# Performance work log

Measured on AMD Instinct MI355X. Metric: run time of the kernel, lower is better.

The kernel has to match this reference:

```python
import jax, jax.numpy as jnp
import numpy as np

T = 4096          # total packed tokens
SEG = 512         # segment length (position_ids reset every SEG)
D = 768           # hidden_size
H = 12            # num_attention_heads
DH = D // H       # head_dim = 64
THETA = 160000.0  # global_rope_theta (layer_id=0 -> global attention)


def setup_inputs() -> dict:
    key = jax.random.key(0)
    k1, k2, k3 = jax.random.split(key, 3)
    hidden_states = jax.random.normal(k1, (T, D), dtype=jnp.float32)
    # torch Linear weights stored transposed: here [in, out] for x @ W
    Wqkv = jax.random.normal(k2, (D, 3 * D), dtype=jnp.float32) / np.sqrt(D).astype(np.float32)
    Wo = jax.random.normal(k3, (D, D), dtype=jnp.float32) / np.sqrt(D).astype(np.float32)
    # packed batch: 8 segments of length SEG, position ids restart at 0
    position_ids = (jnp.arange(T, dtype=jnp.int32) % SEG)
    return {"hidden_states": hidden_states, "Wqkv": Wqkv, "Wo": Wo,
            "position_ids": position_ids}


def _neox_rope(x, pos):
    # x: [T, H, DH]; neox-style rotary over full head_dim
    half = DH // 2
    inv_freq = 1.0 / (THETA ** (jnp.arange(half, dtype=jnp.float32) * 2.0 / DH))
    freqs = pos.astype(jnp.float32)[:, None] * inv_freq[None, :]   # [T, half]
    cos = jnp.cos(freqs)[:, None, :]                               # [T, 1, half]
    sin = jnp.sin(freqs)[:, None, :]
    x1, x2 = x[..., :half], x[..., half:]
    return jnp.concatenate([x1 * cos - x2 * sin, x2 * cos + x1 * sin], axis=-1)


def reference(hidden_states, Wqkv, Wo, position_ids):
    qkv = hidden_states @ Wqkv                         # [T, 3D]
    q, k, v = jnp.split(qkv, 3, axis=-1)
    q = q.reshape(T, H, DH)
    k = k.reshape(T, H, DH)
    v = v.reshape(T, H, DH)
    q = _neox_rope(q, position_ids)
    k = _neox_rope(k, position_ids)
    # segment id per token (position_ids==0 marks a new sequence)
    seg = jnp.cumsum((position_ids == 0).astype(jnp.int32)) - 1
    mask = seg[:, None] == seg[None, :]                # block-diagonal [T, T]
    scale = 1.0 / np.sqrt(DH).astype(np.float32)
    scores = jnp.einsum('thd,shd->hts', q, k) * scale  # [H, T, T]
    scores = jnp.where(mask[None, :, :], scores, jnp.float32(-1e30))
    attn = jax.nn.softmax(scores, axis=-1)
    out = jnp.einsum('hts,shd->thd', attn, v).reshape(T, D)
    return out @ Wo
```

## Files before the change

### kernel.cpp

```cpp
#include <hip/hip_runtime.h>
#include <hip/hip_bf16.h>
#include <math.h>

#define T_TOK 4096
#define D_MODEL 768
#define H_HEADS 12
#define DH 64
#define SEG 512
#define NSEG 8
#define QKV_LD 2304

typedef __bf16 bf16x8_t __attribute__((ext_vector_type(8)));
typedef float f32x4_t __attribute__((ext_vector_type(4)));
typedef float f32x16_t __attribute__((ext_vector_type(16)));

#define GBK 64

#define FENCED_BARRIER()                         \
    do {                                         \
        __builtin_amdgcn_sched_barrier(0);       \
        __builtin_amdgcn_s_barrier();            \
        __builtin_amdgcn_sched_barrier(0);       \
    } while (0)

__device__ __forceinline__ void tconv_body(const float* __restrict__ in,
                                           __hip_bfloat16* __restrict__ out,
                                           int N, int K, int bx, int by, int tid,
                                           float (*tile)[65]) {
    const int k0 = by * 64;
    const int n0 = bx * 64;
    const int rr = tid >> 4;
    const int cc = (tid & 15) * 4;
#pragma unroll
    for (int i = 0; i < 4; ++i) {
        int r = i * 16 + rr;
        float4 v = *(const float4*)(in + (size_t)(k0 + r) * N + n0 + cc);
        tile[r][cc] = v.x; tile[r][cc + 1] = v.y; tile[r][cc + 2] = v.z; tile[r][cc + 3] = v.w;
    }
    __syncthreads();
#pragma unroll
    for (int i = 0; i < 4; ++i) {
        int n = i * 16 + rr;
        union { __hip_bfloat16 h[4]; ushort4 u; } o;
        o.h[0] = __float2bfloat16(tile[cc + 0][n]);
        o.h[1] = __float2bfloat16(tile[cc + 1][n]);
        o.h[2] = __float2bfloat16(tile[cc + 2][n]);
        o.h[3] = __float2bfloat16(tile[cc + 3][n]);
        *(ushort4*)(out + (size_t)(n0 + n) * K + k0 + cc) = o.u;
    }
}

__global__ __launch_bounds__(256) void prep_inputs(const float* __restrict__ hidden,
                                                   const float* __restrict__ Wqkv,
                                                   const float* __restrict__ Wo,
                                                   __hip_bfloat16* __restrict__ Xb,
                                                   __hip_bfloat16* __restrict__ Wqkvt,
                                                   __hip_bfloat16* __restrict__ Wot) {
    __shared__ float tile[64][65];
    const int b = blockIdx.x;
    const int tid = threadIdx.x;
    if (b < 3072) {
        int i = b * 256 + tid;
        float4 v = ((const float4*)hidden)[i];
        union { __hip_bfloat16 h[4]; ushort4 u; } o;
        o.h[0] = __float2bfloat16(v.x); o.h[1] = __float2bfloat16(v.y);
        o.h[2] = __float2bfloat16(v.z); o.h[3] = __float2bfloat16(v.w);
        ((ushort4*)Xb)[i] = o.u;
    } else if (b < 3504) {
        int lb = b - 3072;
        tconv_body(Wqkv, Wqkvt, QKV_LD, D_MODEL, lb % 36, lb / 36, tid, tile);
    } else {
        int lb = b - 3504;
        tconv_body(Wo, Wot, D_MODEL, D_MODEL, lb % 12, lb / 12, tid, tile);
    }
}

__global__ __launch_bounds__(512) void gemm_qkv_fused(const __hip_bfloat16* __restrict__ A,
                                                      const __hip_bfloat16* __restrict__ Bt,
                                                      const int* __restrict__ pos_ids,
                                                      __hip_bfloat16* __restrict__ Qb,
                                                      __hip_bfloat16* __restrict__ Kb,
                                                      __hip_bfloat16* __restrict__ Vtb) {
    __shared__ __hip_bfloat16 As[2][128 * GBK];
    __shared__ __hip_bfloat16 Bs[2][128 * GBK];
    const int tid = threadIdx.x;
    const int lane = tid & 63;
    const int wid = tid >> 6;
    const int wr = wid >> 1;
    const int wc = wid & 1;
    const int m0 = blockIdx.y * 128;
    const int n0 = blockIdx.x * 128;
    const int K = D_MODEL;

    f32x4_t acc[2][4];
#pragma unroll
    for (int i = 0; i < 2; ++i)
#pragma unroll
        for (int j = 0; j < 4; ++j) acc[i][j] = (f32x4_t){0.f, 0.f, 0.f, 0.f};

    const int lr = lane >> 3;
    const int gc = lane & 7;
    const int swzc = (gc ^ lr) << 3;
    const int fr = lane & 15;
    const int l4 = lane >> 4;
    const int fsw = fr & 7;

#define STAGE_Q(buf_, k0_)                                                            \
    do {                                                                              \
        _Pragma("unroll")                                                             \
        for (int i_ = 0; i_ < 2; ++i_) {                                              \
            const int row_ = i_ * 64 + wid * 8;                                       \
            const __hip_bfloat16* ga_ = A + (size_t)(m0 + row_ + lr) * K + (k0_) + swzc; \
            __builtin_amdgcn_global_load_lds(                                         \
                (const __attribute__((address_space(1))) void*)ga_,                   \
                (__attribute__((address_space(3))) void*)(As[buf_] + row_ * GBK), 16, 0, 0); \
            const __hip_bfloat16* gb_ = Bt + (size_t)(n0 + row_ + lr) * K + (k0_) + swzc; \
            __builtin_amdgcn_global_load_lds(                                         \
                (const __attribute__((address_space(1))) void*)gb_,                   \
                (__attribute__((address_space(3))) void*)(Bs[buf_] + row_ * GBK), 16, 0, 0); \
        }                                                                             \
    } while (0)

    const int NKT = K / GBK;
    STAGE_Q(0, 0);
    for (int kt = 0; kt < NKT; ++kt) {
        const int cur = kt & 1;
        if (kt < NKT - 1) {
            STAGE_Q(cur ^ 1, (kt + 1) * GBK);
            asm volatile("s_waitcnt vmcnt(4)" ::: "memory");
        } else {
            asm volatile("s_waitcnt vmcnt(0)" ::: "memory");
        }
        FENCED_BARRIER();
#pragma unroll
        for (int kk = 0; kk < 2; ++kk) {
            const int rg = ((kk * 4 + l4) ^ fsw) << 3;
            bf16x8_t af[2], bfr[4];
#pragma unroll
            for (int mi = 0; mi < 2; ++mi)
                af[mi] = *(const bf16x8_t*)(As[cur] + (wr * 32 + mi * 16 + fr) * GBK + rg);
#pragma unroll
            for (int ni = 0; ni < 4; ++ni)
                bfr[ni] = *(const bf16x8_t*)(Bs[cur] + (wc * 64 + ni * 16 + fr) * GBK + rg);
#pragma unroll
            for (int mi = 0; mi < 2; ++mi)
#pragma unroll
                for (int ni = 0; ni < 4; ++ni)
                    acc[mi][ni] = __builtin_amdgcn_mfma_f32_16x16x32_bf16(
                        af[mi], bfr[ni], acc[mi][ni], 0, 0, 0);
        }
        asm volatile("" ::: "memory");
        FENCED_BARRIER();
    }
#undef STAGE_Q

    const int colbase = n0 + wc * 64;
    const int chunk = colbase >> 6;
    const int part = chunk / H_HEADS;
    const int h = chunk % H_HEADS;
    const int trow0 = m0 + wr * 32;

    if (part == 2) {
        const int seg = trow0 >> 9;
        const int key0 = (trow0 & 511) + l4 * 4;
        __hip_bfloat16* vdst = Vtb + ((size_t)(h * NSEG + seg) * DH) * SEG;
#pragma unroll
        for (int mi = 0; mi < 2; ++mi)
#pragma unroll
            for (int ni = 0; ni < 4; ++ni) {
                int d = ni * 16 + fr;
                union { __hip_bfloat16 h2[4]; ushort4 u; } o;
#pragma unroll
                for (int j = 0; j < 4; ++j) o.h2[j] = __float2bfloat16(acc[mi][ni][j]);
                *(ushort4*)(vdst + (size_t)d * SEG + key0 + mi * 16) = o.u;
            }
    } else {
        __hip_bfloat16* dst = (part == 0) ? Qb : Kb;
        const float scale = (part == 0) ? 0.125f : 1.0f;
        const float if0 = powf(160000.0f, -(float)fr / 32.0f);
        const float if1 = powf(160000.0f, -(float)(16 + fr) / 32.0f);
#pragma unroll
        for (int mi = 0; mi < 2; ++mi)
#pragma unroll
            for (int j = 0; j < 4; ++j) {
                int t = trow0 + mi * 16 + l4 * 4 + j;
                float pos = (float)pos_ids[t];
                float s0, c0, s1, c1;
                sincosf(pos * if0, &s0, &c0);
                sincosf(pos * if1, &s1, &c1);
                __hip_bfloat16* op = dst + ((size_t)h * T_TOK + t) * DH;
                float x1, x2;
                x1 = acc[mi][0][j]; x2 = acc[mi][2][j];
                op[fr]      = __float2bfloat16((x1 * c0 - x2 * s0) * scale);
                op[fr + 32] = __float2bfloat16((x2 * c0 + x1 * s0) * scale);
                x1 = acc[mi][1][j]; x2 = acc[mi][3][j];
                op[16 + fr] = __float2bfloat16((x1 * c1 - x2 * s1) * scale);
                op[48 + fr] = __float2bfloat16((x2 * c1 + x1 * s1) * scale);
            }
    }
}

__global__ __launch_bounds__(256) void gemm_wo64(const __hip_bfloat16* __restrict__ A,
                                                 const __hip_bfloat16* __restrict__ Bt,
                                                 float* __restrict__ C) {
    __shared__ __hip_bfloat16 As[2][64 * GBK];
    __shared__ __hip_bfloat16 Bs[2][64 * GBK];
    const int tid = threadIdx.x;
    const int lane = tid & 63;
    const int wid = tid >> 6;
    const int wr = wid >> 1, wc = wid & 1;
    const int m0 = blockIdx.y * 64;
    const int n0 = blockIdx.x * 64;
    const int K = D_MODEL;
    const int N = D_MODEL;

    f32x4_t acc[2][2];
#pragma unroll
    for (int i = 0; i < 2; ++i)
#pragma unroll
        for (int j = 0; j < 2; ++j) acc[i][j] = (f32x4_t){0.f, 0.f, 0.f, 0.f};

    const int lr = lane >> 3;
    const int gc = lane & 7;
    const int swzc = (gc ^ lr) << 3;
    const int fr = lane & 15;
    const int l4 = lane >> 4;
    const int fsw = fr & 7;

#define STAGE_W(buf_, k0_)                                                            \
    do {                                                                              \
        _Pragma("unroll")                                                             \
        for (int i_ = 0; i_ < 2; ++i_) {                                              \
            const int row_ = i_ * 32 + wid * 8;                                       \
            const __hip_bfloat16* ga_ = A + (size_t)(m0 + row_ + lr) * K + (k0_) + swzc; \
            __builtin_amdgcn_global_load_lds(                                         \
                (const __attribute__((address_space(1))) void*)ga_,                   \
                (__attribute__((address_space(3))) void*)(As[buf_] + row_ * GBK), 16, 0, 0); \
            const __hip_bfloat16* gb_ = Bt + (size_t)(n0 + row_ + lr) * K + (k0_) + swzc; \
            __builtin_amdgcn_global_load_lds(                                         \
                (const __attribute__((address_space(1))) void*)gb_,                   \
                (__attribute__((address_space(3))) void*)(Bs[buf_] + row_ * GBK), 16, 0, 0); \
        }                                                                             \
    } while (0)

    const int NKT = K / GBK;
    STAGE_W(0, 0);
    for (int kt = 0; kt < NKT; ++kt) {
        const int cur = kt & 1;
        if (kt < NKT - 1) {
            STAGE_W(cur ^ 1, (kt + 1) * GBK);
            asm volatile("s_waitcnt vmcnt(4)" ::: "memory");
        } else {
            asm volatile("s_waitcnt vmcnt(0)" ::: "memory");
        }
        FENCED_BARRIER();
#pragma unroll
        for (int kk = 0; kk < 2; ++kk) {
            const int rg = ((kk * 4 + l4) ^ fsw) << 3;
            bf16x8_t af[2], bfr[2];
#pragma unroll
            for (int mi = 0; mi < 2; ++mi)
                af[mi] = *(const bf16x8_t*)(As[cur] + (wr * 32 + mi * 16 + fr) * GBK + rg);
#pragma unroll
            for (int ni = 0; ni < 2; ++ni)
                bfr[ni] = *(const bf16x8_t*)(Bs[cur] + (wc * 32 + ni * 16 + fr) * GBK + rg);
#pragma unroll
            for (int mi = 0; mi < 2; ++mi)
#pragma unroll
                for (int ni = 0; ni < 2; ++ni)
                    acc[mi][ni] = __builtin_amdgcn_mfma_f32_16x16x32_bf16(
                        af[mi], bfr[ni], acc[mi][ni], 0, 0, 0);
        }
        asm volatile("" ::: "memory");
        FENCED_BARRIER();
    }
#undef STAGE_W

    float* Cb = C + (size_t)(m0 + wr * 32) * N + n0 + wc * 32;
#pragma unroll
    for (int mi = 0; mi < 2; ++mi)
#pragma unroll
        for (int ni = 0; ni < 2; ++ni)
#pragma unroll
            for (int j = 0; j < 4; ++j) {
                int r = mi * 16 + (lane >> 4) * 4 + j;
                Cb[(size_t)r * N + ni * 16 + fr] = acc[mi][ni][j];
            }
}

__device__ __forceinline__ unsigned pk2(float a, float b) {
    unsigned ua = (unsigned)__bfloat16_as_ushort(__float2bfloat16(a));
    unsigned ub = (unsigned)__bfloat16_as_ushort(__float2bfloat16(b));
    return ua | (ub << 16);
}

__global__ __launch_bounds__(128) void attn_mfma(const __hip_bfloat16* __restrict__ Qb,
                                                 const __hip_bfloat16* __restrict__ Kb,
                                                 const __hip_bfloat16* __restrict__ Vtb,
                                                 __hip_bfloat16* __restrict__ attnb) {
    __shared__ __hip_bfloat16 KS[2][64 * 64];
    __shared__ __hip_bfloat16 VS[2][64 * 64];

    const int tid = threadIdx.x;
    const int lane = tid & 63;
    const int w = tid >> 6;
    const int hi = lane >> 5;
    const int l31 = lane & 31;
    const int qt = blockIdx.x, h = blockIdx.y, seg = blockIdx.z;
    const int t0 = seg * SEG + qt * 64 + w * 32;

    const __hip_bfloat16* kb = Kb + ((size_t)h * T_TOK + seg * SEG) * DH;
    const __hip_bfloat16* vb = Vtb + (size_t)(h * NSEG + seg) * DH * SEG;

    bf16x8_t qf[4];
    {
        const __hip_bfloat16* qp = Qb + ((size_t)h * T_TOK + t0 + l31) * DH + hi * 8;
#pragma unroll
        for (int s = 0; s < 4; ++s) qf[s] = *(const bf16x8_t*)(qp + s * 16);
    }

    const int gr = lane >> 3;
    const int gc = lane & 7;

#pragma unroll
    for (int i = 0; i < 4; ++i) {
        int G = i * 128 + w * 64;
        int rk = (G >> 3) + gr;
        const __hip_bfloat16* sk = kb + (size_t)rk * DH + ((gc ^ (rk & 7)) << 3);
        __builtin_amdgcn_global_load_lds(
            (const __attribute__((address_space(1))) void*)sk,
            (__attribute__((address_space(3))) void*)(&KS[0][G * 8]), 16, 0, 0);
        const __hip_bfloat16* sv = vb + (size_t)rk * SEG + ((gc ^ (rk & 7)) << 3);
        __builtin_amdgcn_global_load_lds(
            (const __attribute__((address_space(1))) void*)sv,
            (__attribute__((address_space(3))) void*)(&VS[0][G * 8]), 16, 0, 0);
    }
    __syncthreads();

    f32x16_t ot[2];
#pragma unroll
    for (int n = 0; n < 2; ++n)
#pragma unroll
        for (int r = 0; r < 16; ++r) ot[n][r] = 0.f;
    float mrun = -3.0e38f, lrun = 0.f;

    for (int kv = 0; kv < 8; ++kv) {
        const int bb = kv & 1;
        if (kv < 7) {
#pragma unroll
            for (int i = 0; i < 4; ++i) {
                int G = i * 128 + w * 64;
                int rk = (G >> 3) + gr;
                const __hip_bfloat16* sk = kb + (size_t)((kv + 1) * 64 + rk) * DH + ((gc ^ (rk & 7)) << 3);
                __builtin_amdgcn_global_load_lds(
                    (const __attribute__((address_space(1))) void*)sk,
                    (__attribute__((address_space(3))) void*)(&KS[bb ^ 1][G * 8]), 16, 0, 0);
                const __hip_bfloat16* sv = vb + (size_t)rk * SEG + (kv + 1) * 64 + ((gc ^ (rk & 7)) << 3);
                __builtin_amdgcn_global_load_lds(
                    (const __attribute__((address_space(1))) void*)sv,
                    (__attribute__((address_space(3))) void*)(&VS[bb ^ 1][G * 8]), 16, 0, 0);
            }
        }

        f32x16_t st[2];
#pragma unroll
        for (int t = 0; t < 2; ++t)
#pragma unroll
            for (int r = 0; r < 16; ++r) st[t][r] = 0.f;
#pragma unroll
        for (int s = 0; s < 4; ++s) {
            int gk = s * 2 + hi;
            bf16x8_t k0 = *(const bf16x8_t*)(&KS[bb][l31 * 64 + ((gk ^ (l31 & 7)) << 3)]);
            bf16x8_t k1 = *(const bf16x8_t*)(&KS[bb][(32 + l31) * 64 + ((gk ^ (l31 & 7)) << 3)]);
            st[0] = __builtin_amdgcn_mfma_f32_32x32x16_bf16(k0, qf[s], st[0], 0, 0, 0);
            st[1] = __builtin_amdgcn_mfma_f32_32x32x16_bf16(k1, qf[s], st[1], 0, 0, 0);
        }

        float tmax = st[0][0];
#pragma unroll
        for (int r = 1; r < 16; ++r) tmax = fmaxf(tmax, st[0][r]);
#pragma unroll
        for (int r = 0; r < 16; ++r) tmax = fmaxf(tmax, st[1][r]);
        tmax = fmaxf(tmax, __shfl_xor(tmax, 32));
        float mnew = fmaxf(mrun, tmax);
        float corr = __expf(mrun - mnew);
        mrun = mnew;
        float psum = 0.f;
#pragma unroll
        for (int t = 0; t < 2; ++t)
#pragma unroll
            for (int r = 0; r < 16; ++r) {
                float p = __expf(st[t][r] - mnew);
                st[t][r] = p;
                psum += p;
            }
        psum += __shfl_xor(psum, 32);
        lrun = lrun * corr + psum;
#pragma unroll
        for (int n = 0; n < 2; ++n)
#pragma unroll
            for (int r = 0; r < 16; ++r) ot[n][r] *= corr;

        bf16x8_t pf[4];
#pragma unroll
        for (int t = 0; t < 2; ++t) {
            unsigned wv[8], ov[8];
#pragma unroll
            for (int j = 0; j < 8; ++j) wv[j] = pk2(st[t][2 * j], st[t][2 * j + 1]);
#pragma unroll
            for (int j = 0; j < 8; ++j) ov[j] = (unsigned)__shfl_xor((int)wv[j], 32);
#pragma unroll
            for (int sh = 0; sh < 2; ++sh) {
                int b = sh * 4;
                union { unsigned u[4]; bf16x8_t v; } u8;
                u8.u[0] = hi ? ov[b + 2] : wv[b + 0];
                u8.u[1] = hi ? ov[b + 3] : wv[b + 1];
                u8.u[2] = hi ? wv[b + 2] : ov[b + 0];
                u8.u[3] = hi ? wv[b + 3] : ov[b + 1];
                pf[t * 2 + sh] = u8.v;
            }
        }

#pragma unroll
        for (int s = 0; s < 4; ++s) {
            int gk = s * 2 + hi;
            bf16x8_t v0 = *(const bf16x8_t*)(&VS[bb][l31 * 64 + ((gk ^ (l31 & 7)) << 3)]);
            bf16x8_t v1 = *(const bf16x8_t*)(&VS[bb][(32 + l31) * 64 + ((gk ^ (l31 & 7)) << 3)]);
            ot[0] = __builtin_amdgcn_mfma_f32_32x32x16_bf16(v0, pf[s], ot[0], 0, 0, 0);
            ot[1] = __builtin_amdgcn_mfma_f32_32x32x16_bf16(v1, pf[s], ot[1], 0, 0, 0);
        }
        __syncthreads();
    }

    float invl = 1.0f / lrun;
    ushort* Os = (ushort*)&KS[0][0];
    const int wbase = w * (64 * 33);
#pragma unroll
    for (int n = 0; n < 2; ++n)
#pragma unroll
        for (int r = 0; r < 16; ++r) {
            int d = n * 32 + (r & 3) + 8 * (r >> 2) + 4 * hi;
            Os[wbase + d * 33 + l31] = __bfloat16_as_ushort(__float2bfloat16(ot[n][r] * invl));
        }
    __syncthreads();
    {
        unsigned ow2[16];
#pragma unroll
        for (int j = 0; j < 16; ++j) {
            unsigned lo = Os[wbase + (hi * 32 + 2 * j) * 33 + l31];
            unsigned hh = Os[wbase + (hi * 32 + 2 * j + 1) * 33 + l31];
            ow2[j] = lo | (hh << 16);
        }
        uint4* gd = (uint4*)(attnb + (size_t)(t0 + l31) * D_MODEL + h * DH + hi * 32);
        gd[0] = make_uint4(ow2[0], ow2[1], ow2[2], ow2[3]);
        gd[1] = make_uint4(ow2[4], ow2[5], ow2[6], ow2[7]);
        gd[2] = make_uint4(ow2[8], ow2[9], ow2[10], ow2[11]);
        gd[3] = make_uint4(ow2[12], ow2[13], ow2[14], ow2[15]);
    }
}

extern "C" void kernel_launch(void* const* d_in, const int* in_sizes, int n_in,
                              void* d_out, int out_size, void* d_ws, size_t ws_size,
                              hipStream_t stream) {
    const float* hidden = (const float*)d_in[0];
    const float* Wqkv   = (const float*)d_in[1];
    const float* Wo     = (const float*)d_in[2];
    const int*   pos    = (const int*)d_in[3];

    char* ws = (char*)d_ws;
    __hip_bfloat16* Xb    = (__hip_bfloat16*)(ws);
    __hip_bfloat16* Wqkvt = (__hip_bfloat16*)(ws + 6291456);
    __hip_bfloat16* Wot   = (__hip_bfloat16*)(ws + 9830400);
    __hip_bfloat16* Qb    = (__hip_bfloat16*)(ws + 11010048);
    __hip_bfloat16* Kb    = (__hip_bfloat16*)(ws + 17301504);
    __hip_bfloat16* Vtb   = (__hip_bfloat16*)(ws + 23592960);
    __hip_bfloat16* attnb = (__hip_bfloat16*)(ws + 29884416);
    float* out = (float*)d_out;

    prep_inputs<<<3648, 256, 0, stream>>>(hidden, Wqkv, Wo, Xb, Wqkvt, Wot);

    gemm_qkv_fused<<<dim3(QKV_LD / 128, T_TOK / 128), 512, 0, stream>>>(
        Xb, Wqkvt, pos, Qb, Kb, Vtb);

    attn_mfma<<<dim3(8, H_HEADS, NSEG), 128, 0, stream>>>(Qb, Kb, Vtb, attnb);

    gemm_wo64<<<dim3(D_MODEL / 64, T_TOK / 64), 256, 0, stream>>>(
        attnb, Wot, out);
}
```

Measured before the change: 79.83 us.

## Use exp2 softmax with lazy rescaling and XCD-aware block remapping

Folds log2(e) into the Q scale so the attention softmax uses exp2f, and skips the running-max rescale of the output accumulator unless the new tile max exceeds the old one by more than 8 (in log2 units). All three kernels remap the linear workgroup id so that blocks sharing operands are grouped on the same XCD, which is meant to improve L2 reuse. The lazy rescale removes per-tile multiplies and an exp but lets unnormalized values grow by up to 2^8, which costs some precision headroom.

```diff
diff --git a/kernel.cpp b/kernel.cpp
--- a/kernel.cpp
+++ b/kernel.cpp
@@ -15,6 +15,7 @@
 typedef float f32x16_t __attribute__((ext_vector_type(16)));
 
 #define GBK 64
+#define QSCALE 0.18033688011112042f
 
 #define FENCED_BARRIER()                         \
     do {                                         \
@@ -88,8 +89,10 @@
     const int wid = tid >> 6;
     const int wr = wid >> 1;
     const int wc = wid & 1;
-    const int m0 = blockIdx.y * 128;
-    const int n0 = blockIdx.x * 128;
+    const int orig = blockIdx.y * 18 + blockIdx.x;
+    const int wg = (orig & 7) * 72 + (orig >> 3);
+    const int m0 = (wg / 18) * 128;
+    const int n0 = (wg % 18) * 128;
     const int K = D_MODEL;
 
     f32x4_t acc[2][4];
@@ -176,7 +179,7 @@
             }
     } else {
         __hip_bfloat16* dst = (part == 0) ? Qb : Kb;
-        const float scale = (part == 0) ? 0.125f : 1.0f;
+        const float scale = (part == 0) ? QSCALE : 1.0f;
         const float if0 = powf(160000.0f, -(float)fr / 32.0f);
         const float if1 = powf(160000.0f, -(float)(16 + fr) / 32.0f);
 #pragma unroll
@@ -209,8 +212,10 @@
     const int lane = tid & 63;
     const int wid = tid >> 6;
     const int wr = wid >> 1, wc = wid & 1;
-    const int m0 = blockIdx.y * 64;
-    const int n0 = blockIdx.x * 64;
+    const int orig = blockIdx.y * 12 + blockIdx.x;
+    const int wg = (orig & 7) * 96 + (orig >> 3);
+    const int m0 = (wg / 12) * 64;
+    const int n0 = (wg % 12) * 64;
     const int K = D_MODEL;
     const int N = D_MODEL;
 
@@ -306,7 +311,12 @@
     const int w = tid >> 6;
     const int hi = lane >> 5;
     const int l31 = lane & 31;
-    const int qt = blockIdx.x, h = blockIdx.y, seg = blockIdx.z;
+    const int orig = blockIdx.x;
+    const int wg = (orig & 7) * 96 + (orig >> 3);
+    const int qt = wg & 7;
+    const int hs = wg >> 3;
+    const int h = hs % H_HEADS;
+    const int seg = hs / H_HEADS;
     const int t0 = seg * SEG + qt * 64 + w * 32;
 
     const __hip_bfloat16* kb = Kb + ((size_t)h * T_TOK + seg * SEG) * DH;
@@ -382,24 +392,28 @@
 #pragma unroll
         for (int r = 0; r < 16; ++r) tmax = fmaxf(tmax, st[1][r]);
         tmax = fmaxf(tmax, __shfl_xor(tmax, 32));
-        float mnew = fmaxf(mrun, tmax);
-        float corr = __expf(mrun - mnew);
-        mrun = mnew;
+
+        if (!__all(tmax <= mrun + 8.0f)) {
+            float mnew = fmaxf(mrun, tmax);
+            float corr = exp2f(mrun - mnew);
+            lrun *= corr;
+#pragma unroll
+            for (int n = 0; n < 2; ++n)
+#pragma unroll
+                for (int r = 0; r < 16; ++r) ot[n][r] *= corr;
+            mrun = mnew;
+        }
         float psum = 0.f;
 #pragma unroll
         for (int t = 0; t < 2; ++t)
 #pragma unroll
             for (int r = 0; r < 16; ++r) {
-                float p = __expf(st[t][r] - mnew);
+                float p = exp2f(st[t][r] - mrun);
                 st[t][r] = p;
                 psum += p;
             }
         psum += __shfl_xor(psum, 32);
-        lrun = lrun * corr + psum;
-#pragma unroll
-        for (int n = 0; n < 2; ++n)
-#pragma unroll
-            for (int r = 0; r < 16; ++r) ot[n][r] *= corr;
+        lrun += psum;
 
         bf16x8_t pf[4];
 #pragma unroll
@@ -482,7 +496,7 @@
     gemm_qkv_fused<<<dim3(QKV_LD / 128, T_TOK / 128), 512, 0, stream>>>(
         Xb, Wqkvt, pos, Qb, Kb, Vtb);
 
-    attn_mfma<<<dim3(8, H_HEADS, NSEG), 128, 0, stream>>>(Qb, Kb, Vtb, attnb);
+    attn_mfma<<<768, 128, 0, stream>>>(Qb, Kb, Vtb, attnb);
 
     gemm_wo64<<<dim3(D_MODEL / 64, T_TOK / 64), 256, 0, stream>>>(
         attnb, Wot, out);
```

Result: faster. 77.18 us (-3.3%).
